# Optimization experiments

Hardware: AMD Instinct MI355X
Metric: run time of the kernel (lower is better)

The kernel has to match this reference:

```python
import jax, jax.numpy as jnp
import numpy as np

HID = 4096
OUT = 4096
L = 64
R = 64
B = 4
S = 2048
QMAX = 7.0  # int4 symmetric range [-8, 7], scale uses 7


def _quantize_weight(key, out_f, in_f):
    # Mimics weight_quantizer.find_params + quantize(quantonly=True):
    # symmetric per-output-channel int4 quantization.
    w = jax.random.normal(key, (out_f, in_f), dtype=jnp.float32) * 0.02
    s = jnp.maximum(jnp.max(jnp.abs(w), axis=1) / QMAX, 1e-8)  # [out]
    wq = jnp.clip(jnp.round(w / s[:, None]), -8.0, 7.0).astype(jnp.int8)
    return wq, s


def setup_inputs() -> dict:
    key = jax.random.key(0)
    ks = jax.random.split(key, 8)
    # FlatQuant learned invertible transforms; use orthogonal init via QR
    ml = jnp.linalg.qr(jax.random.normal(ks[0], (L, L), dtype=jnp.float32))[0]
    mr = jnp.linalg.qr(jax.random.normal(ks[1], (R, R), dtype=jnp.float32))[0]
    wq, sq = _quantize_weight(ks[2], OUT, HID)
    wk, sk = _quantize_weight(ks[3], OUT, HID)
    wv, sv = _quantize_weight(ks[4], OUT, HID)
    hs = jax.random.normal(ks[5], (B, S, HID), dtype=jnp.float32)
    return {
        "hidden_states": hs,
        "left_trans": ml.T,  # module stores matrix_left.T
        "right_trans": mr,
        "wt_q": wq, "scale_q": sq,
        "wt_k": wk, "scale_k": sk,
        "wt_v": wv, "scale_v": sv,
    }


def _flat_quant_linear(x, left, right, w_int, w_scale):
    # AscendW4A4FlatQuantDynamicLinearMethod.apply:
    # 1) two-sided Kronecker transform on the hidden dim (H = L*R)
    # 2) dynamic per-token symmetric int4 activation quantization
    b, s, h = x.shape
    l = left.shape[0]
    r = right.shape[0]
    xr = x.reshape(b, s, l, r)
    xt = jnp.einsum('ml,bslr,rn->bsmn', left, xr, right).reshape(b, s, h)
    a_scale = jnp.maximum(jnp.max(jnp.abs(xt), axis=-1, keepdims=True) / QMAX, 1e-8)  # [b,s,1]
    xq = jnp.clip(jnp.round(xt / a_scale), -8.0, 7.0)
    y = jnp.einsum('bsh,oh->bso', xq, w_int.astype(jnp.float32))
    return y * a_scale * w_scale[None, None, :]


def reference(hidden_states, left_trans, right_trans, wt_q, scale_q, wt_k, scale_k, wt_v, scale_v):
    b, s, _ = hidden_states.shape
    pad = 0
    if (b % 16) and (s % 16):  # static shapes -> Python control flow is fine
        pad = (s // 16 + 1) * 16 - s
        hidden_states = jnp.pad(hidden_states, ((0, 0), (0, pad), (0, 0)))
    wq = wt_q.astype(jnp.int8) if wt_q.dtype != jnp.int8 else wt_q
    wk = wt_k.astype(jnp.int8) if wt_k.dtype != jnp.int8 else wt_k
    wv = wt_v.astype(jnp.int8) if wt_v.dtype != jnp.int8 else wt_v
    q = _flat_quant_linear(hidden_states, left_trans, right_trans, wq, scale_q)
    k = _flat_quant_linear(hidden_states, left_trans, right_trans, wk, scale_k)
    v = _flat_quant_linear(hidden_states, left_trans, right_trans, wv, scale_v)
    if pad:
        q, k, v = q[:, :s], k[:, :s], v[:, :s]
    return q, k, v
```

## Files before the change

### kernel.cpp

```cpp
#include <hip/hip_runtime.h>

#define HID   4096
#define OUTF  4096
#define NTOK  8192
#define PROJ_STRIDE 33554432ull

typedef int   i32x4 __attribute__((ext_vector_type(4)));
typedef float f32x4 __attribute__((ext_vector_type(4)));

__global__ __launch_bounds__(256) void cvt_weights_i8(const int* __restrict__ w,
                                                      char* __restrict__ o,
                                                      int n4) {
    int i = blockIdx.x * blockDim.x + threadIdx.x;
    if (i < n4) {
        int4 v = ((const int4*)w)[i];
        int packed = (v.x & 255) | ((v.y & 255) << 8) |
                     ((v.z & 255) << 16) | (v.w << 24);
        ((int*)o)[i] = packed;
    }
}

__global__ __launch_bounds__(256) void transpose64(const float* __restrict__ in,
                                                   float* __restrict__ out) {
    int i = blockIdx.x * 256 + threadIdx.x;
    int r = i >> 6, c = i & 63;
    out[c * 64 + r] = in[i];
}

__global__ __launch_bounds__(256) void transform_quant(
    const float* __restrict__ hs, const float* __restrict__ leftT,
    const float* __restrict__ right, char* __restrict__ xq,
    float* __restrict__ ascale) {
    __shared__ __align__(16) float Xs[4096];
    __shared__ __align__(16) float Ls[4096];
    __shared__ __align__(16) float Rs[4096];
    __shared__ float red[256];

    const int t   = blockIdx.x;
    const int tid = threadIdx.x;
    const int tm  = tid >> 4;
    const int tn  = tid & 15;

    {
        const float* src = hs + (size_t)t * HID;
        #pragma unroll
        for (int i = 0; i < 4; i++) {
            int c = tid + i * 256;
            __builtin_amdgcn_global_load_lds(
                (const __attribute__((address_space(1))) void*)(src + c * 4),
                (__attribute__((address_space(3))) void*)(Xs + c * 4), 16, 0, 0);
            __builtin_amdgcn_global_load_lds(
                (const __attribute__((address_space(1))) void*)(leftT + c * 4),
                (__attribute__((address_space(3))) void*)(Ls + c * 4), 16, 0, 0);
            __builtin_amdgcn_global_load_lds(
                (const __attribute__((address_space(1))) void*)(right + c * 4),
                (__attribute__((address_space(3))) void*)(Rs + c * 4), 16, 0, 0);
        }
    }
    __syncthreads();

    float acc[4][4];
    #pragma unroll
    for (int i = 0; i < 4; i++)
        #pragma unroll
        for (int j = 0; j < 4; j++) acc[i][j] = 0.f;

    #pragma unroll 4
    for (int l = 0; l < 64; l++) {
        f32x4 xv = *(const f32x4*)(Xs + l * 64 + tn * 4);
        f32x4 lv = *(const f32x4*)(Ls + l * 64 + tm * 4);
        #pragma unroll
        for (int i = 0; i < 4; i++)
            #pragma unroll
            for (int j = 0; j < 4; j++)
                acc[i][j] = fmaf(lv[i], xv[j], acc[i][j]);
    }
    __syncthreads();

    #pragma unroll
    for (int j = 0; j < 4; j++) {
        int r = tn * 4 + j;
        int q = tm ^ (r & 7);
        f32x4 col = {acc[0][j], acc[1][j], acc[2][j], acc[3][j]};
        *(f32x4*)(Xs + r * 64 + q * 4) = col;
    }
    __syncthreads();

    #pragma unroll
    for (int i = 0; i < 4; i++)
        #pragma unroll
        for (int j = 0; j < 4; j++) acc[i][j] = 0.f;
    #pragma unroll 4
    for (int r = 0; r < 64; r++) {
        f32x4 rv = *(const f32x4*)(Rs + r * 64 + tn * 4);
        int q = tm ^ (r & 7);
        f32x4 tv = *(const f32x4*)(Xs + r * 64 + q * 4);
        #pragma unroll
        for (int i = 0; i < 4; i++)
            #pragma unroll
            for (int j = 0; j < 4; j++)
                acc[i][j] = fmaf(tv[i], rv[j], acc[i][j]);
    }

    float mx = 0.f;
    #pragma unroll
    for (int i = 0; i < 4; i++)
        #pragma unroll
        for (int j = 0; j < 4; j++) mx = fmaxf(mx, fabsf(acc[i][j]));
    red[tid] = mx;
    __syncthreads();
    for (int s = 128; s > 0; s >>= 1) {
        if (tid < s) red[tid] = fmaxf(red[tid], red[tid + s]);
        __syncthreads();
    }
    float scale = fmaxf(red[0] * (1.0f / 7.0f), 1e-8f);

    char* dst = xq + (size_t)t * HID;
    #pragma unroll
    for (int i = 0; i < 4; i++) {
        int packed = 0;
        #pragma unroll
        for (int j = 0; j < 4; j++) {
            float q = rintf(acc[i][j] / scale);
            q = fminf(fmaxf(q, -8.f), 7.f);
            packed |= ((int)q & 255) << (8 * j);
        }
        *(int*)(dst + (tm * 4 + i) * 64 + tn * 4) = packed;
    }
    if (tid == 0) ascale[t] = scale;
}

#define BM 128
#define BN 128
#define BKI 64

__global__ __launch_bounds__(256) void gemm_qkv(
    const char* __restrict__ xq, const float* __restrict__ ascale,
    const char* __restrict__ w8, const float* __restrict__ sq,
    const float* __restrict__ sk, const float* __restrict__ sv,
    float* __restrict__ out) {
    __shared__ __align__(16) char As[BM * BKI];
    __shared__ __align__(16) char Bs[BN * BKI];

    const int tid  = threadIdx.x;
    const int lane = tid & 63;
    const int wave = tid >> 6;
    const int wr   = wave >> 1;
    const int wc   = wave & 1;
    const int ml   = lane & 15;
    const int kq   = lane >> 4;

    const int mb   = blockIdx.x;
    const int proj = blockIdx.y >> 5;
    const int nb   = blockIdx.y & 31;

    const char* wp = w8 + (size_t)proj * ((size_t)OUTF * HID);
    const float* wscale = (proj == 0) ? sq : ((proj == 1) ? sk : sv);

    const size_t rowA0 = (size_t)mb * BM;
    const size_t rowB0 = (size_t)nb * BN;

    i32x4 acc[4][4];
    #pragma unroll
    for (int i = 0; i < 4; i++)
        #pragma unroll
        for (int j = 0; j < 4; j++) {
            i32x4 z = {0, 0, 0, 0};
            acc[i][j] = z;
        }

    for (int k0 = 0; k0 < HID; k0 += BKI) {
        #pragma unroll
        for (int tch = 0; tch < 2; tch++) {
            int c   = tid + tch * 256;
            int row = c >> 2, kc = c & 3;
            const char* g = xq + (rowA0 + row) * HID + k0 + kc * 16;
            __builtin_amdgcn_global_load_lds(
                (const __attribute__((address_space(1))) void*)g,
                (__attribute__((address_space(3))) void*)(As + c * 16), 16, 0, 0);
        }
        #pragma unroll
        for (int tch = 0; tch < 2; tch++) {
            int c   = tid + tch * 256;
            int row = c >> 2, kc = c & 3;
            const char* g = wp + (rowB0 + row) * HID + k0 + kc * 16;
            __builtin_amdgcn_global_load_lds(
                (const __attribute__((address_space(1))) void*)g,
                (__attribute__((address_space(3))) void*)(Bs + c * 16), 16, 0, 0);
        }
        __syncthreads();

        i32x4 af[4], bfr[4];
        #pragma unroll
        for (int i = 0; i < 4; i++)
            af[i] = *(const i32x4*)(As + (wr * 64 + i * 16 + ml) * BKI + kq * 16);
        #pragma unroll
        for (int j = 0; j < 4; j++)
            bfr[j] = *(const i32x4*)(Bs + (wc * 64 + j * 16 + ml) * BKI + kq * 16);

        #pragma unroll
        for (int i = 0; i < 4; i++)
            #pragma unroll
            for (int j = 0; j < 4; j++)
                acc[i][j] = __builtin_amdgcn_mfma_i32_16x16x64_i8(
                    af[i], bfr[j], acc[i][j], 0, 0, 0);
        __syncthreads();
    }

    #pragma unroll
    for (int i = 0; i < 4; i++) {
        #pragma unroll
        for (int rg = 0; rg < 4; rg++) {
            int row  = mb * BM + wr * 64 + i * 16 + kq * 4 + rg;
            float as = ascale[row];
            #pragma unroll
            for (int j = 0; j < 4; j++) {
                int col = nb * BN + wc * 64 + j * 16 + ml;
                out[(size_t)proj * PROJ_STRIDE + (size_t)row * OUTF + col] =
                    (float)acc[i][j][rg] * as * wscale[col];
            }
        }
    }
}

extern "C" void kernel_launch(void* const* d_in, const int* in_sizes, int n_in,
                              void* d_out, int out_size, void* d_ws, size_t ws_size,
                              hipStream_t stream) {
    const float* hs    = (const float*)d_in[0];
    const float* left  = (const float*)d_in[1];
    const float* right = (const float*)d_in[2];
    const int*   wq    = (const int*)d_in[3];
    const float* sq    = (const float*)d_in[4];
    const int*   wk    = (const int*)d_in[5];
    const float* sk    = (const float*)d_in[6];
    const int*   wv    = (const int*)d_in[7];
    const float* sv    = (const float*)d_in[8];
    float* out = (float*)d_out;

    char*  xq8  = (char*)d_ws;
    float* ascl = (float*)((char*)d_ws + 33554432ull);
    char*  w8   = (char*)d_ws + 33587200ull;
    float* ltT  = (float*)((char*)d_ws + 83918848ull);

    const int nW = OUTF * HID;
    const int n4 = nW / 4;
    dim3 cblk(256), cgrd((n4 + 255) / 256);
    cvt_weights_i8<<<cgrd, cblk, 0, stream>>>(wq, w8 + 0ull * (size_t)nW, n4);
    cvt_weights_i8<<<cgrd, cblk, 0, stream>>>(wk, w8 + 1ull * (size_t)nW, n4);
    cvt_weights_i8<<<cgrd, cblk, 0, stream>>>(wv, w8 + 2ull * (size_t)nW, n4);

    transpose64<<<dim3(16), dim3(256), 0, stream>>>(left, ltT);

    transform_quant<<<dim3(NTOK), dim3(256), 0, stream>>>(hs, ltT, right, xq8, ascl);

    gemm_qkv<<<dim3(NTOK / BM, 3 * (OUTF / BN)), dim3(256), 0, stream>>>(
        xq8, ascl, w8, sq, sk, sv, out);
}
```

Measured before the change: 1.237 ms.

## Rewrite int8 QKV GEMM with 256x256 tiles, double-buffered LDS and swizzling

Replaces the simple 128x128 single-buffered GEMM with a 256x256x128 tile, 512-thread kernel that stages global-to-LDS loads into a double buffer across eight interleaved compute phases. It uses vmcnt gating and s_setprio so memory prefetch overlaps MFMA work. LDS addresses are XOR-swizzled to avoid bank conflicts, and workgroup IDs are remapped for L2 locality. The larger tiles raise register pressure and LDS use (128KB per block), and the hand-scheduled barriers make correctness fragile.

Result: faster. 1.193 ms (-3.5%).

```diff
diff --git a/kernel.cpp b/kernel.cpp
--- a/kernel.cpp
+++ b/kernel.cpp
@@ -130,94 +130,134 @@
     if (tid == 0) ascale[t] = scale;
 }
 
-#define BM 128
-#define BN 128
-#define BKI 64
-
-__global__ __launch_bounds__(256) void gemm_qkv(
+#define BM 256
+#define BN 256
+#define BKI 128
+#define NIT 16
+
+#define STAGE(GB, R0, KT, DREG)                                              \
+  { _Pragma("unroll") for (int jj_ = 0; jj_ < 2; jj_++) {                    \
+      const int c_  = jj_ * 512 + tid;                                       \
+      const int rh_ = c_ >> 3;                                               \
+      const int sw_ = ((c_ ^ rh_) & 7) << 4;                                 \
+      const char* g_ = (GB) + (size_t)((R0) + rh_) * HID + (KT) * BKI + sw_; \
+      __builtin_amdgcn_global_load_lds(                                      \
+          (const __attribute__((address_space(1))) void*)g_,                 \
+          (__attribute__((address_space(3))) void*)((DREG) + c_ * 16),       \
+          16, 0, 0);                                                         \
+  } }
+
+#define PHASE(QM, QN, BUF, PF_STMT, GATE_STMT)                               \
+  {                                                                          \
+    const char* Ab_ = As + (BUF) * 32768 + (QM) * 16384;                     \
+    const char* Bb_ = Bs + (BUF) * 32768 + (QN) * 16384;                     \
+    i32x4 a0_[4], a1_[4], b0_[2], b1_[2];                                    \
+    _Pragma("unroll") for (int ii = 0; ii < 4; ii++) {                       \
+      const int rh = wr * 64 + ii * 16 + ml;                                 \
+      const int bs = rh * 128 + kq * 16;                                     \
+      a0_[ii] = *(const i32x4*)(Ab_ + ((bs) ^ xr));                          \
+      a1_[ii] = *(const i32x4*)(Ab_ + ((bs + 64) ^ xr));                     \
+    }                                                                        \
+    _Pragma("unroll") for (int jj = 0; jj < 2; jj++) {                       \
+      const int rh = wc * 32 + jj * 16 + ml;                                 \
+      const int bs = rh * 128 + kq * 16;                                     \
+      b0_[jj] = *(const i32x4*)(Bb_ + ((bs) ^ xr));                          \
+      b1_[jj] = *(const i32x4*)(Bb_ + ((bs + 64) ^ xr));                     \
+    }                                                                        \
+    PF_STMT;                                                                 \
+    GATE_STMT;                                                               \
+    __builtin_amdgcn_sched_barrier(0);                                       \
+    __builtin_amdgcn_s_barrier();                                            \
+    __builtin_amdgcn_s_setprio(1);                                           \
+    _Pragma("unroll") for (int ii = 0; ii < 4; ii++)                         \
+      _Pragma("unroll") for (int jj = 0; jj < 2; jj++) {                     \
+        acc[(QM)*4+ii][(QN)*2+jj] = __builtin_amdgcn_mfma_i32_16x16x64_i8(   \
+            a0_[ii], b0_[jj], acc[(QM)*4+ii][(QN)*2+jj], 0, 0, 0);           \
+        acc[(QM)*4+ii][(QN)*2+jj] = __builtin_amdgcn_mfma_i32_16x16x64_i8(   \
+            a1_[ii], b1_[jj], acc[(QM)*4+ii][(QN)*2+jj], 0, 0, 0);           \
+      }                                                                      \
+    __builtin_amdgcn_s_setprio(0);                                           \
+    __builtin_amdgcn_sched_barrier(0);                                       \
+    __builtin_amdgcn_s_barrier();                                            \
+    __builtin_amdgcn_sched_barrier(0);                                       \
+  }
+
+#define GATE4 if (pf) { asm volatile("s_waitcnt vmcnt(4)" ::: "memory"); } \
+              else    { asm volatile("s_waitcnt vmcnt(0)" ::: "memory"); }
+
+__global__ __launch_bounds__(512, 2) void gemm_qkv(
     const char* __restrict__ xq, const float* __restrict__ ascale,
     const char* __restrict__ w8, const float* __restrict__ sq,
     const float* __restrict__ sk, const float* __restrict__ sv,
     float* __restrict__ out) {
-    __shared__ __align__(16) char As[BM * BKI];
-    __shared__ __align__(16) char Bs[BN * BKI];
+    __shared__ __align__(16) char As[2 * 2 * 16384];
+    __shared__ __align__(16) char Bs[2 * 2 * 16384];
 
     const int tid  = threadIdx.x;
     const int lane = tid & 63;
     const int wave = tid >> 6;
-    const int wr   = wave >> 1;
-    const int wc   = wave & 1;
+    const int wr   = wave >> 2;
+    const int wc   = wave & 3;
     const int ml   = lane & 15;
     const int kq   = lane >> 4;
-
-    const int mb   = blockIdx.x;
-    const int proj = blockIdx.y >> 5;
-    const int nb   = blockIdx.y & 31;
-
-    const char* wp = w8 + (size_t)proj * ((size_t)OUTF * HID);
+    const int xr   = (ml & 7) << 4;
+
+    const int wg   = blockIdx.x;
+    const int swz  = (wg & 7) * 192 + (wg >> 3);
+    const int proj = swz >> 9;
+    const int rr   = swz & 511;
+    const int nb   = rr >> 5;
+    const int mb   = rr & 31;
+
+    const char* Ag = xq;
+    const char* Bg = w8 + (size_t)proj * ((size_t)OUTF * HID);
     const float* wscale = (proj == 0) ? sq : ((proj == 1) ? sk : sv);
 
     const size_t rowA0 = (size_t)mb * BM;
     const size_t rowB0 = (size_t)nb * BN;
 
-    i32x4 acc[4][4];
-    #pragma unroll
-    for (int i = 0; i < 4; i++)
+    i32x4 acc[8][4];
+    #pragma unroll
+    for (int i = 0; i < 8; i++)
         #pragma unroll
         for (int j = 0; j < 4; j++) {
             i32x4 z = {0, 0, 0, 0};
             acc[i][j] = z;
         }
 
-    for (int k0 = 0; k0 < HID; k0 += BKI) {
-        #pragma unroll
-        for (int tch = 0; tch < 2; tch++) {
-            int c   = tid + tch * 256;
-            int row = c >> 2, kc = c & 3;
-            const char* g = xq + (rowA0 + row) * HID + k0 + kc * 16;
-            __builtin_amdgcn_global_load_lds(
-                (const __attribute__((address_space(1))) void*)g,
-                (__attribute__((address_space(3))) void*)(As + c * 16), 16, 0, 0);
-        }
-        #pragma unroll
-        for (int tch = 0; tch < 2; tch++) {
-            int c   = tid + tch * 256;
-            int row = c >> 2, kc = c & 3;
-            const char* g = wp + (rowB0 + row) * HID + k0 + kc * 16;
-            __builtin_amdgcn_global_load_lds(
-                (const __attribute__((address_space(1))) void*)g,
-                (__attribute__((address_space(3))) void*)(Bs + c * 16), 16, 0, 0);
-        }
-        __syncthreads();
-
-        i32x4 af[4], bfr[4];
-        #pragma unroll
-        for (int i = 0; i < 4; i++)
-            af[i] = *(const i32x4*)(As + (wr * 64 + i * 16 + ml) * BKI + kq * 16);
-        #pragma unroll
-        for (int j = 0; j < 4; j++)
-            bfr[j] = *(const i32x4*)(Bs + (wc * 64 + j * 16 + ml) * BKI + kq * 16);
-
-        #pragma unroll
-        for (int i = 0; i < 4; i++)
-            #pragma unroll
-            for (int j = 0; j < 4; j++)
-                acc[i][j] = __builtin_amdgcn_mfma_i32_16x16x64_i8(
-                    af[i], bfr[j], acc[i][j], 0, 0, 0);
-        __syncthreads();
-    }
-
-    #pragma unroll
-    for (int i = 0; i < 4; i++) {
+    STAGE(Ag, rowA0,       0, As + 0);
+    STAGE(Bg, rowB0,       0, Bs + 0);
+    STAGE(Ag, rowA0 + 128, 0, As + 16384);
+    STAGE(Bg, rowB0 + 128, 0, Bs + 16384);
+    STAGE(Ag, rowA0,       1, As + 32768);
+    STAGE(Bg, rowB0,       1, Bs + 32768);
+    asm volatile("s_waitcnt vmcnt(4)" ::: "memory");
+    __builtin_amdgcn_s_barrier();
+
+    for (int t = 0; t < NIT; t++) {
+        const bool pf = (t < NIT - 1);
+        const int k1 = 2 * t + 1, k2 = 2 * t + 2, k3 = 2 * t + 3;
+        PHASE(0, 0, 0, STAGE(Ag, rowA0 + 128, k1, As + 32768 + 16384), ;)
+        PHASE(0, 1, 0, STAGE(Bg, rowB0 + 128, k1, Bs + 32768 + 16384), ;)
+        PHASE(1, 0, 0, if (pf) STAGE(Ag, rowA0,       k2, As + 0), ;)
+        PHASE(1, 1, 0, if (pf) STAGE(Bg, rowB0,       k2, Bs + 0), GATE4)
+        PHASE(0, 0, 1, if (pf) STAGE(Ag, rowA0 + 128, k2, As + 16384), ;)
+        PHASE(0, 1, 1, if (pf) STAGE(Bg, rowB0 + 128, k2, Bs + 16384), ;)
+        PHASE(1, 0, 1, if (pf) STAGE(Ag, rowA0,       k3, As + 32768), ;)
+        PHASE(1, 1, 1, if (pf) STAGE(Bg, rowB0,       k3, Bs + 32768), GATE4)
+    }
+
+    #pragma unroll
+    for (int i = 0; i < 8; i++) {
+        const int row = (int)rowA0 + (i >> 2) * 128 + wr * 64 + (i & 3) * 16 + kq * 4;
         #pragma unroll
         for (int rg = 0; rg < 4; rg++) {
-            int row  = mb * BM + wr * 64 + i * 16 + kq * 4 + rg;
-            float as = ascale[row];
+            const float as = ascale[row + rg];
+            float* orow = out + (size_t)proj * PROJ_STRIDE + (size_t)(row + rg) * OUTF;
             #pragma unroll
             for (int j = 0; j < 4; j++) {
-                int col = nb * BN + wc * 64 + j * 16 + ml;
-                out[(size_t)proj * PROJ_STRIDE + (size_t)row * OUTF + col] =
-                    (float)acc[i][j][rg] * as * wscale[col];
+                const int col = (int)rowB0 + (j >> 1) * 128 + wc * 32 + (j & 1) * 16 + ml;
+                orow[col] = (float)acc[i][j][rg] * as * wscale[col];
             }
         }
     }
@@ -253,6 +293,6 @@
 
     transform_quant<<<dim3(NTOK), dim3(256), 0, stream>>>(hs, ltT, right, xq8, ascl);
 
-    gemm_qkv<<<dim3(NTOK / BM, 3 * (OUTF / BN)), dim3(256), 0, stream>>>(
+    gemm_qkv<<<dim3((NTOK / BM) * (OUTF / BN) * 3), dim3(512), 0, stream>>>(
         xq8, ascl, w8, sq, sk, sv, out);
 }
```
